# Kernel tuning notes

Measured on AMD Instinct MI355X. Metric: run time of the kernel, lower is better.

The kernel has to match this reference:

```python
import jax, jax.numpy as jnp
import numpy as np

D_MODEL = 1024
NUM_HEADS = 16
D_K = D_MODEL // NUM_HEADS
LN_EPS = 1e-5
NEG = -1e9


def setup_inputs() -> dict:
    key = jax.random.key(0)
    ks = jax.random.split(key, 12)
    B, S, D = 8, 1024, D_MODEL
    lim = 1.0 / np.sqrt(D)
    def lin(k):
        k1, k2 = jax.random.split(k)
        W = jax.random.uniform(k1, (D, D), jnp.float32, -lim, lim)
        b = jax.random.uniform(k2, (D,), jnp.float32, -lim, lim)
        return W, b
    Wq, bq = lin(ks[0])
    Wk, bk = lin(ks[1])
    Wv, bv = lin(ks[2])
    Wo, bo = lin(ks[3])
    return {
        "history_items": jax.random.normal(ks[4], (B, S, D), jnp.float32),
        "sequence_mask": jax.random.randint(ks[5], (B, S), 0, 2, jnp.int32),
        "Wq": Wq, "bq": bq, "Wk": Wk, "bk": bk,
        "Wv": Wv, "bv": bv, "Wo": Wo, "bo": bo,
        "ln_gamma": jnp.ones((D,), jnp.float32),
        "ln_beta": jnp.zeros((D,), jnp.float32),
    }


def reference(history_items, sequence_mask, Wq, bq, Wk, bk, Wv, bv, Wo, bo, ln_gamma, ln_beta):
    B, S, D = history_items.shape
    H, dk = NUM_HEADS, D_K
    # projections -> [B, H, S, dk]
    def proj(W, b):
        return (history_items @ W.T + b).reshape(B, S, H, dk).transpose(0, 2, 1, 3)
    q = proj(Wq, bq)
    k = proj(Wk, bk)
    v = proj(Wv, bv)
    # combined mask: causal [1,1,S,S] AND key-padding [B,1,1,S]
    causal = jnp.tril(jnp.ones((S, S), bool))[None, None]
    mask = jnp.logical_and(causal, (sequence_mask != 0)[:, None, None, :])
    scores = jnp.einsum('bhqd,bhkd->bhqk', q, k) / np.sqrt(dk).astype(np.float32)
    scores = jnp.where(mask, scores, NEG)
    attn = jax.nn.softmax(scores, axis=-1)
    ctx = jnp.einsum('bhqk,bhkd->bhqd', attn, v)  # [B,H,S,dk]
    concat = ctx.transpose(0, 2, 1, 3).reshape(B, S, D)
    out = concat @ Wo.T + bo
    x = out + history_items
    mu = jnp.mean(x, axis=-1, keepdims=True)
    var = jnp.mean((x - mu) ** 2, axis=-1, keepdims=True)
    return (x - mu) * jax.lax.rsqrt(var + LN_EPS) * ln_gamma + ln_beta
```

## Files before the change

### kernel.cpp

```cpp
#include <hip/hip_runtime.h>
#include <hip/hip_bf16.h>

#define B_ 8
#define S_ 1024
#define D_ 1024
#define H_ 16
#define DK_ 64
#define M_ (B_*S_)

#define QSCALE 0.1803368801111904f

typedef __attribute__((ext_vector_type(4))) float f32x4;
typedef __attribute__((ext_vector_type(8))) short bf16x8;
typedef __attribute__((ext_vector_type(4))) short s16x4;
typedef __hip_bfloat16 bf16;
typedef unsigned long long ull;

#define GLOAD_LDS16(gp, lp) __builtin_amdgcn_global_load_lds( \
    (const __attribute__((address_space(1))) void*)(gp), \
    (__attribute__((address_space(3))) void*)(lp), 16, 0, 0)

__device__ __forceinline__ bf16x8 ld8(const bf16* p){ return *(const bf16x8*)p; }

__device__ __forceinline__ short bf16bits(float f){
  bf16 h = __float2bfloat16(f);
  return __builtin_bit_cast(short, h);
}
__device__ __forceinline__ float tof(short b){
  unsigned u = ((unsigned)(unsigned short)b) << 16;
  return __builtin_bit_cast(float, u);
}

__device__ __forceinline__ bf16x8 ld8swz(const bf16* base, int row, int colb){
  int sw = colb ^ ((row & 7) << 4);
  return *(const bf16x8*)((const char*)base + row*128 + sw);
}

template<int CTRL>
__device__ __forceinline__ float dppadd(float x){
  int m = __builtin_amdgcn_update_dpp(0, __builtin_bit_cast(int,x), CTRL, 0xF, 0xF, true);
  return x + __builtin_bit_cast(float,m);
}
__device__ __forceinline__ float red16add(float x){
  x = dppadd<0xB1>(x);
  x = dppadd<0x4E>(x);
  x = dppadd<0x141>(x);
  x = dppadd<0x140>(x);
  return x;
}

__global__ __launch_bounds__(256) void cast_f32_bf16(const float* __restrict__ in,
                                                     bf16* __restrict__ out, int n){
  int i = (blockIdx.x*256 + threadIdx.x)*8;
  if (i >= n) return;
  f32x4 a = *(const f32x4*)(in+i);
  f32x4 b = *(const f32x4*)(in+i+4);
  bf16x8 o;
  #pragma unroll
  for (int c=0;c<4;c++){ o[c] = bf16bits(a[c]); o[c+4] = bf16bits(b[c]); }
  *(bf16x8*)(out+i) = o;
}

__global__ __launch_bounds__(256) void cast_w4(const float* __restrict__ w0, const float* __restrict__ w1,
                                               const float* __restrict__ w2, const float* __restrict__ w3,
                                               bf16* __restrict__ out){
  int sel = blockIdx.x >> 9;
  const float* src = (sel==0)?w0:((sel==1)?w1:((sel==2)?w2:w3));
  int i = (((blockIdx.x & 511)*256) + threadIdx.x)*8;
  f32x4 a = *(const f32x4*)(src+i);
  f32x4 b = *(const f32x4*)(src+i+4);
  bf16x8 o;
  #pragma unroll
  for (int c=0;c<4;c++){ o[c] = bf16bits(a[c]); o[c+4] = bf16bits(b[c]); }
  *(bf16x8*)(out + ((size_t)sel<<20) + i) = o;
}

__global__ __launch_bounds__(256) void vmean_kernel(const bf16* __restrict__ Vt_g,
                                                    float* __restrict__ vmean){
  int r = blockIdx.x*4 + (threadIdx.x>>6);
  int lane = threadIdx.x & 63;
  const bf16* p = Vt_g + (((size_t)r)<<10) + lane*16;
  bf16x8 a = ld8(p), c = ld8(p+8);
  float s = 0.f;
  #pragma unroll
  for (int e=0;e<8;e++) s += tof(a[e]) + tof(c[e]);
  #pragma unroll
  for (int off=1;off<64;off<<=1) s += __shfl_xor(s, off);
  if (lane==0) vmean[r] = s * (1.f/1024.f);
}

template<int MODE>
__global__ __launch_bounds__(256) void gemm128(
    const bf16* __restrict__ A,
    const bf16* __restrict__ W0, const bf16* __restrict__ W1, const bf16* __restrict__ W2,
    const float* __restrict__ b0, const float* __restrict__ b1, const float* __restrict__ b2,
    bf16* __restrict__ o0, bf16* __restrict__ o1, bf16* __restrict__ o2,
    const float* __restrict__ resid, float* __restrict__ xout)
{
  const bf16* Wsel = W0; const float* bsel = b0;
  if (MODE==0){
    int z = blockIdx.z;
    Wsel = (z==0)?W0:((z==1)?W1:W2);
    bsel = (z==0)?b0:((z==1)?b1:b2);
  }
  __shared__ bf16 smem[2*128*64];
  bf16* As = smem;
  bf16* Bs = smem + 128*64;
  const int tid = threadIdx.x, wid = tid>>6, lane = tid&63;
  const int lr = lane&15, lg = lane>>4;
  const int m0 = blockIdx.x*128, n0 = blockIdx.y*128;
  const int wr = wid>>1, wc = wid&1;
  f32x4 acc[4][4] = {};

  for (int k0=0; k0<1024; k0+=64){
    __syncthreads();
    #pragma unroll
    for (int c=0;c<4;c++){
      int ldsoff = ((c<<2)|wid)<<10;
      int off = ldsoff + (lane<<4);
      int row = off>>7;
      int colb = (off&127) ^ ((row&7)<<4);
      GLOAD_LDS16(A   + (((size_t)(m0+row))<<10) + k0 + (colb>>1), (char*)As + ldsoff);
      GLOAD_LDS16(Wsel+ (((size_t)(n0+row))<<10) + k0 + (colb>>1), (char*)Bs + ldsoff);
    }
    __syncthreads();
    bf16x8 af[4][2], bfv[4][2];
    #pragma unroll
    for (int m=0;m<4;m++){
      int row = wr*64 + m*16 + lr;
      af[m][0] = ld8swz(As, row, lg*16);
      af[m][1] = ld8swz(As, row, lg*16 + 64);
    }
    #pragma unroll
    for (int n=0;n<4;n++){
      int row = wc*64 + n*16 + lr;
      bfv[n][0] = ld8swz(Bs, row, lg*16);
      bfv[n][1] = ld8swz(Bs, row, lg*16 + 64);
    }
    #pragma unroll
    for (int m=0;m<4;m++)
      #pragma unroll
      for (int n=0;n<4;n++){
        acc[m][n] = __builtin_amdgcn_mfma_f32_16x16x32_bf16(af[m][0], bfv[n][0], acc[m][n],0,0,0);
        acc[m][n] = __builtin_amdgcn_mfma_f32_16x16x32_bf16(af[m][1], bfv[n][1], acc[m][n],0,0,0);
      }
  }

  if (MODE==0){
    if (blockIdx.z == 2){
      __syncthreads();
      #pragma unroll
      for (int n=0;n<4;n++){
        int c = wc*64 + n*16 + lr;
        float bias = bsel[n0 + c];
        #pragma unroll
        for (int m=0;m<4;m++){
          int r0 = wr*64 + m*16 + lg*4;
          s16x4 pk;
          #pragma unroll
          for (int j=0;j<4;j++) pk[j] = bf16bits(acc[m][n][j] + bias);
          *(s16x4*)((char*)smem + c*256 + ((r0*2) ^ ((c&7)<<4))) = pk;
        }
      }
      __syncthreads();
      #pragma unroll
      for (int q=0;q<8;q++){
        int idx = tid + q*256;
        int c = idx>>4, r8 = idx&15;
        bf16x8 vv = *(const bf16x8*)((char*)smem + c*256 + ((r8*16) ^ ((c&7)<<4)));
        int col = n0 + c;  int h = col>>6, dd = col&63;
        int row0 = m0 + r8*8;  int bb = row0>>10, s0 = row0&1023;
        *(bf16x8*)(o2 + ((((size_t)bb*H_ + h)*DK_ + dd)<<10) + s0) = vv;
      }
    } else {
      bf16* osel = (blockIdx.z==0) ? o0 : o1;
      const float qs = (blockIdx.z==0) ? QSCALE : 1.0f;
      #pragma unroll
      for (int n=0;n<4;n++){
        int col = n0 + wc*64 + n*16 + lr;
        float bias = bsel[col];
        int h = col>>6, dd = col&63;
        #pragma unroll
        for (int m=0;m<4;m++)
          #pragma unroll
          for (int j=0;j<4;j++){
            int row = m0 + wr*64 + m*16 + lg*4 + j;
            int bb = row>>10, s = row&1023;
            osel[((((size_t)bb*H_ + h)<<10) + s)*DK_ + dd] = __float2bfloat16((acc[m][n][j] + bias)*qs);
          }
      }
    }
  } else {
    #pragma unroll
    for (int n=0;n<4;n++){
      int col = n0 + wc*64 + n*16 + lr;
      float bias = bsel[col];
      #pragma unroll
      for (int m=0;m<4;m++)
        #pragma unroll
        for (int j=0;j<4;j++){
          int row = m0 + wr*64 + m*16 + lg*4 + j;
          size_t idx = (((size_t)row)<<10) + col;
          xout[idx] = acc[m][n][j] + bias + resid[idx];
        }
    }
  }
}

__global__ __launch_bounds__(512) void attn_kernel(
    const bf16* __restrict__ Q, const bf16* __restrict__ K, const bf16* __restrict__ Vt_g,
    const int* __restrict__ seqm, const float* __restrict__ vmean, bf16* __restrict__ ctxout)
{
  __shared__ bf16 Ks[2][64*64];
  __shared__ bf16 Vs[2][64*64];
  __shared__ bf16 Ps[8][32*72];
  __shared__ int msk[1024];
  const int tid = threadIdx.x, wid = tid>>6, lane = tid&63;
  const int lr = lane&15, lg = lane>>4;
  const int bh = blockIdx.x, xb = blockIdx.y;
  const int b = bh>>4, h = bh&15;
  const bf16* Qb  = Q    + (size_t)bh * S_ * DK_;
  const bf16* Kb  = K    + (size_t)bh * S_ * DK_;
  const bf16* Vtb = Vt_g + (size_t)bh * DK_ * S_;
  for (int i=tid;i<1024;i+=512) msk[i] = seqm[b*1024+i];

  const int g0 = 8*xb + wid;
  const int rb0 = g0*16;
  const int rb1 = (63 - g0)*16;
  bf16x8 qf[2][2];
  {
    const bf16* p0 = Qb + (size_t)(rb0+lr)*DK_ + lg*8;
    const bf16* p1 = Qb + (size_t)(rb1+lr)*DK_ + lg*8;
    qf[0][0] = ld8(p0); qf[0][1] = ld8(p0+32);
    qf[1][0] = ld8(p1); qf[1][1] = ld8(p1+32);
  }
  f32x4 cacc[2][4] = {};
  float lsum[2][4] = {};

  auto STAGE = [&](int t, int bsel){
    const int j0 = t*64;
    int off = (wid<<10) + (lane<<4);
    int row = off>>7;
    int colb = (off&127) ^ ((row&7)<<4);
    GLOAD_LDS16(Kb  + (size_t)(j0+row)*DK_ + (colb>>1), (char*)&Ks[bsel][0] + (wid<<10));
    GLOAD_LDS16(Vtb + (((size_t)row)<<10) + j0 + (colb>>1), (char*)&Vs[bsel][0] + (wid<<10));
  };

  STAGE(0, 0);
  __syncthreads();

  ull mbits = 0;
  #pragma unroll
  for (int i=0;i<64;i++) mbits |= ((ull)(msk[i*16+lr]!=0)) << i;

  const int bnt = ((1023 - 128*xb) >> 6) + 1;

  int cur = 0;
  for (int t=0; t<bnt; t++){
    if (t+1 < bnt) STAGE(t+1, cur^1);
    const int j0 = t*64;
    if (j0 <= rb1 + 15){
      const bool act0 = (j0 <= rb0 + 15);
      bf16x8 kf[4][2];
      #pragma unroll
      for (int nf=0;nf<4;nf++){
        kf[nf][0] = ld8swz(&Ks[cur][0], nf*16+lr, lg*16);
        kf[nf][1] = ld8swz(&Ks[cur][0], nf*16+lr, lg*16 + 64);
      }
      float madd[4];
      #pragma unroll
      for (int nf=0;nf<4;nf++)
        madd[nf] = ((mbits >> (t*4 + nf)) & 1ull) ? 0.f : -1.0e9f;

      #pragma unroll
      for (int mf=0;mf<2;mf++){
        if (mf==0 && !act0) continue;
        const int rbm = mf ? rb1 : rb0;
        const bool diag = (j0 + 63 > rbm);
        f32x4 sc[4] = {};
        #pragma unroll
        for (int nf=0;nf<4;nf++){
          sc[nf] = __builtin_amdgcn_mfma_f32_16x16x32_bf16(qf[mf][0], kf[nf][0], sc[nf],0,0,0);
          sc[nf] = __builtin_amdgcn_mfma_f32_16x16x32_bf16(qf[mf][1], kf[nf][1], sc[nf],0,0,0);
        }
        #pragma unroll
        for (int j=0;j<4;j++){
          int row = rbm + lg*4 + j;
          float ps = 0.f;
          #pragma unroll
          for (int nf=0;nf<4;nf++){
            float s = sc[nf][j] + madd[nf];
            if (diag){
              int col = j0 + nf*16 + lr;
              s = (col <= row) ? s : -1.0e9f;
            }
            float p = exp2f(s);
            sc[nf][j] = p;
            ps += p;
          }
          lsum[mf][j] += ps;
        }
        #pragma unroll
        for (int nf=0;nf<4;nf++)
          #pragma unroll
          for (int j=0;j<4;j++)
            Ps[wid][(mf*16+lg*4+j)*72 + nf*16+lr] = __float2bfloat16(sc[nf][j]);
      }
      bf16x8 pf[2][2];
      #pragma unroll
      for (int mf=0;mf<2;mf++){
        if (mf==0 && !act0) continue;
        const bf16* p = &Ps[wid][(mf*16+lr)*72 + lg*8];
        pf[mf][0] = *(const bf16x8*)p; pf[mf][1] = *(const bf16x8*)(p+32);
      }
      #pragma unroll
      for (int df=0;df<4;df++){
        #pragma unroll
        for (int kk=0;kk<2;kk++){
          bf16x8 vf = ld8swz(&Vs[cur][0], df*16+lr, lg*16 + kk*64);
          if (act0)
            cacc[0][df] = __builtin_amdgcn_mfma_f32_16x16x32_bf16(pf[0][kk], vf, cacc[0][df],0,0,0);
          cacc[1][df] = __builtin_amdgcn_mfma_f32_16x16x32_bf16(pf[1][kk], vf, cacc[1][df],0,0,0);
        }
      }
    }
    __syncthreads();
    cur ^= 1;
  }

  #pragma unroll
  for (int mf=0;mf<2;mf++){
    const int rbm = mf ? rb1 : rb0;
    float lt[4];
    #pragma unroll
    for (int j=0;j<4;j++) lt[j] = red16add(lsum[mf][j]);
    #pragma unroll
    for (int df=0;df<4;df++)
      #pragma unroll
      for (int j=0;j<4;j++){
        int srow = rbm + lg*4 + j;
        int dd = df*16 + lr;
        float v = cacc[mf][df][j] / lt[j];
        if (lt[j] <= 1.0e-30f) v = vmean[bh*64 + dd];
        ctxout[((size_t)b*S_ + srow)*D_ + h*DK_ + dd] = __float2bfloat16(v);
      }
  }
}

__global__ __launch_bounds__(256) void ln_kernel(const float* __restrict__ X2,
    const float* __restrict__ gamma, const float* __restrict__ beta, float* __restrict__ out)
{
  const int row = blockIdx.x, tid = threadIdx.x;
  const int lane = tid&63, wid = tid>>6;
  const f32x4* xr = (const f32x4*)(X2 + (((size_t)row)<<10));
  f32x4 v = xr[tid];
  float s  = v[0]+v[1]+v[2]+v[3];
  float s2 = v[0]*v[0]+v[1]*v[1]+v[2]*v[2]+v[3]*v[3];
  #pragma unroll
  for (int off=1;off<64;off<<=1){ s += __shfl_xor(s,off); s2 += __shfl_xor(s2,off); }
  __shared__ float red[8];
  if (lane==0){ red[wid]=s; red[wid+4]=s2; }
  __syncthreads();
  s  = red[0]+red[1]+red[2]+red[3];
  s2 = red[4]+red[5]+red[6]+red[7];
  float mu  = s*(1.f/1024.f);
  float var = s2*(1.f/1024.f) - mu*mu;
  float inv = rsqrtf(var + 1e-5f);
  f32x4 gv = ((const f32x4*)gamma)[tid], bv = ((const f32x4*)beta)[tid];
  f32x4 o;
  #pragma unroll
  for (int c=0;c<4;c++) o[c] = (v[c]-mu)*inv*gv[c] + bv[c];
  ((f32x4*)(out + (((size_t)row)<<10)))[tid] = o;
}

extern "C" void kernel_launch(void* const* d_in, const int* in_sizes, int n_in,
                              void* d_out, int out_size, void* d_ws, size_t ws_size,
                              hipStream_t stream) {
  const float* X   = (const float*)d_in[0];
  const int*   sm  = (const int*)d_in[1];
  const float* Wq  = (const float*)d_in[2];  const float* bq = (const float*)d_in[3];
  const float* Wk  = (const float*)d_in[4];  const float* bk = (const float*)d_in[5];
  const float* Wv  = (const float*)d_in[6];  const float* bv = (const float*)d_in[7];
  const float* Wo  = (const float*)d_in[8];  const float* bo = (const float*)d_in[9];
  const float* ga  = (const float*)d_in[10]; const float* be = (const float*)d_in[11];
  float* out = (float*)d_out;
  char* ws = (char*)d_ws;

  bf16* Xbf = (bf16*)(ws);
  bf16* Wqb = (bf16*)(ws + (16u<<20));
  bf16* Wkb = (bf16*)(ws + (18u<<20));
  bf16* Wvb = (bf16*)(ws + (20u<<20));
  bf16* Wob = (bf16*)(ws + (22u<<20));
  bf16* Qh  = (bf16*)(ws + (24u<<20));
  bf16* Kh  = (bf16*)(ws + (40u<<20));
  bf16* Vth = (bf16*)(ws + (56u<<20));
  bf16* Ctx = (bf16*)(ws + (72u<<20));
  float* X2 = (float*)(ws + (24u<<20));
  float* vmean = (float*)(ws + (16u<<20));

  cast_f32_bf16<<<4096,256,0,stream>>>(X,  Xbf, M_*D_);
  cast_w4<<<2048,256,0,stream>>>(Wq, Wk, Wv, Wo, Wqb);

  dim3 g1(M_/128, D_/128, 3);
  gemm128<0><<<g1,256,0,stream>>>(Xbf, Wqb,Wkb,Wvb, bq,bk,bv, Qh,Kh,Vth, nullptr, nullptr);

  vmean_kernel<<<B_*H_*DK_/4,256,0,stream>>>(Vth, vmean);

  dim3 g2(B_*H_, 4);
  attn_kernel<<<g2,512,0,stream>>>(Qh, Kh, Vth, sm, vmean, Ctx);

  dim3 g3(M_/128, D_/128, 1);
  gemm128<1><<<g3,256,0,stream>>>(Ctx, Wob,nullptr,nullptr, bo,nullptr,nullptr,
                                  nullptr,nullptr,nullptr, X, X2);

  ln_kernel<<<M_,256,0,stream>>>(X2, ga, be, out);
}
```

Measured before the change: 187.6 us.

## Double-buffer GEMM LDS tiles to overlap global loads with MFMA

The 128x128 GEMM kernel now keeps two LDS stages and issues the direct-to-LDS global loads for the next K tile before computing the current one. Manual vmcnt waits and raw s_barrier replace the two __syncthreads per iteration, so memory latency can hide behind MFMA work. LDS use doubles to 64KB per block, which may lower occupancy. It also relies on hand-placed waitcnt and sched barriers being correct.

```diff
diff --git a/kernel.cpp b/kernel.cpp
--- a/kernel.cpp
+++ b/kernel.cpp
@@ -19,6 +19,9 @@
 #define GLOAD_LDS16(gp, lp) __builtin_amdgcn_global_load_lds( \
     (const __attribute__((address_space(1))) void*)(gp), \
     (__attribute__((address_space(3))) void*)(lp), 16, 0, 0)
+
+#define SBAR()   asm volatile("s_barrier" ::: "memory")
+#define VMCNT(n) asm volatile("s_waitcnt vmcnt(" #n ")" ::: "memory")
 
 __device__ __forceinline__ bf16x8 ld8(const bf16* p){ return *(const bf16x8*)p; }
 
@@ -103,39 +106,46 @@
     Wsel = (z==0)?W0:((z==1)?W1:W2);
     bsel = (z==0)?b0:((z==1)?b1:b2);
   }
-  __shared__ bf16 smem[2*128*64];
-  bf16* As = smem;
-  bf16* Bs = smem + 128*64;
+  __shared__ bf16 smem[4*128*64];
   const int tid = threadIdx.x, wid = tid>>6, lane = tid&63;
   const int lr = lane&15, lg = lane>>4;
   const int m0 = blockIdx.x*128, n0 = blockIdx.y*128;
   const int wr = wid>>1, wc = wid&1;
   f32x4 acc[4][4] = {};
 
-  for (int k0=0; k0<1024; k0+=64){
-    __syncthreads();
+  auto STAGE = [&](int k0, int bsel_){
     #pragma unroll
     for (int c=0;c<4;c++){
       int ldsoff = ((c<<2)|wid)<<10;
       int off = ldsoff + (lane<<4);
       int row = off>>7;
       int colb = (off&127) ^ ((row&7)<<4);
-      GLOAD_LDS16(A   + (((size_t)(m0+row))<<10) + k0 + (colb>>1), (char*)As + ldsoff);
-      GLOAD_LDS16(Wsel+ (((size_t)(n0+row))<<10) + k0 + (colb>>1), (char*)Bs + ldsoff);
-    }
-    __syncthreads();
+      GLOAD_LDS16(A   + (((size_t)(m0+row))<<10) + k0 + (colb>>1), (char*)smem + bsel_*32768 + ldsoff);
+      GLOAD_LDS16(Wsel+ (((size_t)(n0+row))<<10) + k0 + (colb>>1), (char*)smem + bsel_*32768 + 16384 + ldsoff);
+    }
+  };
+
+  STAGE(0, 0);
+  int cur = 0;
+  for (int kt=0; kt<16; kt++){
+    if (kt < 15){ STAGE((kt+1)<<6, cur^1); VMCNT(8); }
+    else        { VMCNT(0); }
+    SBAR();
+    __builtin_amdgcn_sched_barrier(0);
+    const bf16* Asb = smem + cur*16384;
+    const bf16* Bsb = Asb + 8192;
     bf16x8 af[4][2], bfv[4][2];
     #pragma unroll
     for (int m=0;m<4;m++){
       int row = wr*64 + m*16 + lr;
-      af[m][0] = ld8swz(As, row, lg*16);
-      af[m][1] = ld8swz(As, row, lg*16 + 64);
+      af[m][0] = ld8swz(Asb, row, lg*16);
+      af[m][1] = ld8swz(Asb, row, lg*16 + 64);
     }
     #pragma unroll
     for (int n=0;n<4;n++){
       int row = wc*64 + n*16 + lr;
-      bfv[n][0] = ld8swz(Bs, row, lg*16);
-      bfv[n][1] = ld8swz(Bs, row, lg*16 + 64);
+      bfv[n][0] = ld8swz(Bsb, row, lg*16);
+      bfv[n][1] = ld8swz(Bsb, row, lg*16 + 64);
     }
     #pragma unroll
     for (int m=0;m<4;m++)
@@ -144,6 +154,9 @@
         acc[m][n] = __builtin_amdgcn_mfma_f32_16x16x32_bf16(af[m][0], bfv[n][0], acc[m][n],0,0,0);
         acc[m][n] = __builtin_amdgcn_mfma_f32_16x16x32_bf16(af[m][1], bfv[n][1], acc[m][n],0,0,0);
       }
+    __builtin_amdgcn_sched_barrier(0);
+    SBAR();
+    cur ^= 1;
   }
 
   if (MODE==0){
```

Measured after the change: 182.1 us. 1.03x faster.
